# Kernel tuning notes

Hardware: AMD Instinct MI355X
Metric: run time of the kernel (lower is better)

The kernel has to match this reference:

```python
import jax, jax.numpy as jnp
import numpy as np

ALPHA = 1.0
BETA = 0.25
NUM_EMBEDS = 8192
EMBED_DIM = 512
B, T = 32, 256


def setup_inputs() -> dict:
    key = jax.random.key(0)
    k1, k2 = jax.random.split(key)
    z_e = jax.random.normal(k1, (B, EMBED_DIM, T), dtype=jnp.float32)
    codebook = jax.random.normal(k2, (NUM_EMBEDS, EMBED_DIM), dtype=jnp.float32)
    return {"z_e": z_e, "codebook": codebook}


def reference(z_e, codebook):
    # z_e: (b, d, t) -> (b, t, d)
    z = jnp.transpose(z_e, (0, 2, 1))
    b, t, d = z.shape
    flat = z.reshape(-1, d)  # (N, d), N = b*t

    # squared euclidean distances to every codebook vector: (N, K)
    dists = (
        jnp.sum(flat * flat, axis=1, keepdims=True)
        + jnp.sum(codebook * codebook, axis=1)
        - 2.0 * flat @ codebook.T
    )
    idx = jnp.argmin(dists, axis=1)  # (N,)

    # codebook lookup (equivalent to one-hot @ codebook)
    z_q = codebook[idx].reshape(b, t, d)

    # commitment loss (codebook is EMA-updated, so only e_latent term)
    e_latent_loss = jnp.mean((jax.lax.stop_gradient(z_q) - z) ** 2)
    vq_loss = ALPHA * BETA * e_latent_loss

    # straight-through estimator
    z_q_st = z + jax.lax.stop_gradient(z_q - z)
    z_q_out = jnp.transpose(z_q_st, (0, 2, 1))  # back to (b, d, t)

    # perplexity from mean one-hot assignment probabilities
    counts = jnp.zeros((codebook.shape[0],), dtype=jnp.float32).at[idx].add(1.0)
    avg_probs = counts / flat.shape[0]
    perplexity = jnp.exp(-jnp.sum(avg_probs * jnp.log(avg_probs + 1e-10)))

    return z_q_out, vq_loss, perplexity
```

## Files before the change

kernel.cpp:

```cpp
#include <hip/hip_runtime.h>
#include <stdint.h>

typedef _Float16 half8 __attribute__((ext_vector_type(8)));
typedef float floatx16 __attribute__((ext_vector_type(16)));
typedef unsigned long long u64;

#define ALPHA_ 1.0f
#define BETA_ 0.25f
#define NUM_EMBEDS 8192
#define EMBED_DIM 512
#define B_ 32
#define T_ 256
#define N_TOK 8192
#define THR_GAP 2e-3f


__device__ __forceinline__ uint32_t mono(float s) {
    uint32_t u = __float_as_uint(s);
    return (u & 0x80000000u) ? ~u : (u | 0x80000000u);
}
__device__ __forceinline__ float unmono(uint32_t v) {
    return __uint_as_float((v & 0x80000000u) ? (v ^ 0x80000000u) : ~v);
}

__global__ void pack_cb_kernel(const float* __restrict__ cb, _Float16* __restrict__ cf,
                               float* __restrict__ cnorm) {
    int row = blockIdx.x * 4 + (threadIdx.x >> 6);
    int l = threadIdx.x & 63;
    const float* src = cb + (size_t)row * EMBED_DIM + l * 8;
    float4 v0 = *(const float4*)src;
    float4 v1 = *(const float4*)(src + 4);
    float x[8] = {v0.x, v0.y, v0.z, v0.w, v1.x, v1.y, v1.z, v1.w};
    half8 hh, mm;
    float s = 0.f;
#pragma unroll
    for (int j = 0; j < 8; ++j) {
        s += x[j] * x[j];
        _Float16 hv = (_Float16)x[j];
        hh[j] = hv;
        mm[j] = (_Float16)((x[j] - (float)hv) * 2048.0f);
    }
    int s_ = l >> 2, kk = (l >> 1) & 1, hfb = l & 1;
    int slot0 = s_ * 4 + kk * 2;
    size_t base = (size_t)(row >> 5) * 32768 + (size_t)slot0 * 512 +
                  (size_t)((row & 31) + hfb * 32) * 8;
    *(half8*)(cf + base) = hh;
    *(half8*)(cf + base + 512) = mm;
#pragma unroll
    for (int d = 32; d; d >>= 1) s += __shfl_xor(s, d, 64);
    if (l == 0) cnorm[row] = s;
}

__global__ void pack_z_kernel(const float* __restrict__ z, _Float16* __restrict__ zf) {
    int tid = threadIdx.x;
    int l = tid & 63, ds = tid >> 6;
    int n = blockIdx.x * 64 + l;
    int b = n >> 8, t = n & 255;
    int kk = ds >> 1, hfb = ds & 1;
    int tb = n >> 7, q = (n >> 5) & 3;
    size_t lanebase = (size_t)tb * 131072 + (size_t)q * 512 +
                      (size_t)((n & 31) + hfb * 32) * 8;
    for (int g = 0; g < 16; ++g) {
        int d0 = g * 32 + ds * 8;
        const float* src = z + ((size_t)b * EMBED_DIM + d0) * T_ + t;
        half8 hh, mm;
#pragma unroll
        for (int j = 0; j < 8; ++j) {
            float x = -2.0f * src[(size_t)j * T_];
            _Float16 hv = (_Float16)x;
            hh[j] = hv;
            mm[j] = (_Float16)((x - (float)hv) * 2048.0f);
        }
        int slot0 = g * 4 + kk * 2;
        _Float16* dst = zf + lanebase + (size_t)slot0 * 2048;
        *(half8*)dst = hh;
        *(half8*)(dst + 2048) = mm;
    }
}

#define MFMA16(a, b, c) __builtin_amdgcn_mfma_f32_32x32x16_f16(a, b, c, 0, 0, 0)

#define LOADSET(X, hs)                                                              \
    X##Ah = *(const half8*)(Ab + ((hs)*2 + 0) * 512 + lane8);                       \
    X##Am = *(const half8*)(Ab + ((hs)*2 + 1) * 512 + lane8);                       \
    _Pragma("unroll") for (int q_ = 0; q_ < 4; ++q_) {                              \
        X##Bh[q_] = *(const half8*)(Bb + (((hs)*2 + 0) * 4 + q_) * 512 + lane8);    \
        X##Bm[q_] = *(const half8*)(Bb + (((hs)*2 + 1) * 4 + q_) * 512 + lane8);    \
    }

#define MFMASET(X)                                                                  \
    _Pragma("unroll") for (int q_ = 0; q_ < 4; ++q_)                                \
        acc1[q_] = MFMA16(X##Ah, X##Bh[q_], acc1[q_]);                              \
    _Pragma("unroll") for (int q_ = 0; q_ < 4; ++q_)                                \
        acc2[q_] = MFMA16(X##Ah, X##Bm[q_], acc2[q_]);                              \
    _Pragma("unroll") for (int q_ = 0; q_ < 4; ++q_)                                \
        acc2[q_] = MFMA16(X##Am, X##Bh[q_], acc2[q_]);

__global__ __launch_bounds__(512, 2) void argmin_kernel(
    const _Float16* __restrict__ cb_f, const _Float16* __restrict__ zt_f,
    const float* __restrict__ cnorm, u64* __restrict__ slot_m1,
    _Float16* __restrict__ slot_d) {
    __shared__ u64 sK[8][128];
    __shared__ float sV1[8][128], sV2[8][128];

    const int tid = threadIdx.x;
    const int l = tid & 63;
    const int wv = tid >> 6;
    const int l31 = l & 31;
    const int hf = l >> 5;
    const int tb = blockIdx.x;
    const int c0 = blockIdx.y * 256;
    const int cb32 = blockIdx.y * 8 + wv;

    const _Float16* Ab = cb_f + (size_t)cb32 * 32768;
    const _Float16* Bb = zt_f + (size_t)tb * 131072;
    const int lane8 = l * 8;

    floatx16 acc1[4], acc2[4];
#pragma unroll
    for (int q = 0; q < 4; ++q)
#pragma unroll
        for (int r = 0; r < 16; ++r) { acc1[q][r] = 0.f; acc2[q][r] = 0.f; }

    half8 cAh, cAm, cBh[4], cBm[4];
    half8 nAh, nAm, nBh[4], nBm[4];

    LOADSET(c, 0);
    for (int hs = 0; hs < 30; hs += 2) {
        LOADSET(n, hs + 1);
        MFMASET(c);
        LOADSET(c, hs + 2);
        MFMASET(n);
    }
    LOADSET(n, 31);
    MFMASET(c);
    MFMASET(n);

    const int cb0 = c0 + wv * 32;
    u64 km[4]; float kv1[4], kv2[4];
#pragma unroll
    for (int q = 0; q < 4; ++q) {
        u64 m1k = ~0ULL;
        float m1v = 3.4e38f, m2 = 3.4e38f;
#pragma unroll
        for (int g = 0; g < 4; ++g) {
            const int cb4 = cb0 + g * 8 + hf * 4;
            float4 cn = *(const float4*)(cnorm + cb4);
            float sv[4] = {cn.x + acc1[q][g * 4 + 0] + acc2[q][g * 4 + 0] * (1.0f / 2048.0f),
                           cn.y + acc1[q][g * 4 + 1] + acc2[q][g * 4 + 1] * (1.0f / 2048.0f),
                           cn.z + acc1[q][g * 4 + 2] + acc2[q][g * 4 + 2] * (1.0f / 2048.0f),
                           cn.w + acc1[q][g * 4 + 3] + acc2[q][g * 4 + 3] * (1.0f / 2048.0f)};
#pragma unroll
            for (int r = 0; r < 4; ++r) {
                u64 key = ((u64)mono(sv[r]) << 32) | (uint32_t)(cb4 + r);
                if (key < m1k) { m2 = m1v; m1v = sv[r]; m1k = key; }
                else m2 = fminf(m2, sv[r]);
            }
        }
        u64 ok = __shfl_xor(m1k, 32, 64);
        float ov = __shfl_xor(m1v, 32, 64);
        float om2 = __shfl_xor(m2, 32, 64);
        if (ok < m1k) { m2 = fminf(fminf(m2, om2), m1v); m1v = ov; m1k = ok; }
        else m2 = fminf(fminf(m2, om2), ov);
        km[q] = m1k; kv1[q] = m1v; kv2[q] = m2;
    }
    if (hf == 0) {
#pragma unroll
        for (int q = 0; q < 4; ++q) {
            int idx = q * 32 + l31;
            sK[wv][idx] = km[q]; sV1[wv][idx] = kv1[q]; sV2[wv][idx] = kv2[q];
        }
    }
    __syncthreads();
    if (tid < 128) {
        u64 m1k = ~0ULL;
        float m1v = 3.4e38f, m2 = 3.4e38f;
#pragma unroll
        for (int w = 0; w < 8; ++w) {
            u64 ok = sK[w][tid]; float ov = sV1[w][tid], om2 = sV2[w][tid];
            if (ok < m1k) { m2 = fminf(fminf(m2, om2), m1v); m1v = ov; m1k = ok; }
            else m2 = fminf(fminf(m2, om2), ov);
        }
        int tok = tb * 128 + tid;
        slot_m1[((size_t)blockIdx.y << 13) + tok] = m1k;
        slot_d[((size_t)blockIdx.y << 13) + tok] = (_Float16)(m2 - m1v);
    }
}

__global__ void combine_kernel(const u64* __restrict__ slot_m1, const _Float16* __restrict__ slot_d,
                               u64* __restrict__ wexact, int* __restrict__ worklist,
                               int* __restrict__ nflag) {
    int tok = blockIdx.x * 256 + threadIdx.x;
    u64 g1 = ~0ULL;
    float g1v = 3.4e38f, g2 = 3.4e38f;
    for (int c = 0; c < 32; ++c) {
        u64 k = slot_m1[((size_t)c << 13) + tok];
        float kv = unmono((uint32_t)(k >> 32));
        float v2 = kv + (float)slot_d[((size_t)c << 13) + tok];
        if (k < g1) { g2 = fminf(g2, g1v); g1 = k; g1v = kv; }
        else g2 = fminf(g2, kv);
        g2 = fminf(g2, v2);
    }
    if (g2 - g1v > THR_GAP) wexact[tok] = g1;
    else { int i = atomicAdd(nflag, 1); if (i < 8192) worklist[i] = tok; }
}

__global__ void fallback_kernel(const float* __restrict__ z, const float* __restrict__ cb,
                                const float* __restrict__ cnorm,
                                const int* __restrict__ worklist, const int* __restrict__ nflag,
                                u64* __restrict__ wexact) {
    int n = *nflag;
    if (n > 8192) n = 8192;
    const int l = threadIdx.x & 63, wv = threadIdx.x >> 6;
    const int cbase = blockIdx.x * 128;
    for (int fi = blockIdx.y; fi < n; fi += gridDim.y) {
        int tok = worklist[fi];
        int b = tok >> 8, t = tok & 255;
        const float* zp = z + ((size_t)b * EMBED_DIM) * T_ + t;
        float zr[8];
#pragma unroll
        for (int j = 0; j < 8; ++j) zr[j] = zp[(size_t)(l * 8 + j) * T_];
        u64 m1 = ~0ULL;
        for (int j = 0; j < 32; ++j) {
            int c = cbase + wv + j * 4;
            const float* cp = cb + (size_t)c * EMBED_DIM + l * 8;
            float4 a = *(const float4*)cp, bb = *(const float4*)(cp + 4);
            float dot = zr[0] * a.x + zr[1] * a.y + zr[2] * a.z + zr[3] * a.w +
                        zr[4] * bb.x + zr[5] * bb.y + zr[6] * bb.z + zr[7] * bb.w;
#pragma unroll
            for (int m = 32; m; m >>= 1) dot += __shfl_xor(dot, m, 64);
            if (l == 0) {
                float s = cnorm[c] - 2.0f * dot;
                u64 key = ((u64)mono(s) << 32) | (uint32_t)c;
                if (key < m1) m1 = key;
            }
        }
        if (l == 0) atomicMin(&wexact[tok], m1);
    }
}

__global__ void gather_kernel(const float* __restrict__ z, const float* __restrict__ cb,
                              const u64* __restrict__ wexact,
                              float* __restrict__ out, int* __restrict__ counts,
                              float* __restrict__ sse_acc) {
    __shared__ unsigned int sIdx[64];
    __shared__ float red[4];
    const int tid = threadIdx.x;
    const int n0 = blockIdx.x * 64;
    const int b = n0 >> 8;
    const int t0 = n0 & 255;
    if (tid < 64) {
        unsigned int idx = (unsigned int)(wexact[n0 + tid] & 0xffffffffULL);
        sIdx[tid] = idx;
        atomicAdd(&counts[idx], 1);
    }
    __syncthreads();
    const int w = tid >> 6;
    const int lane = tid & 63;
    const float* crow = cb + (size_t)sIdx[lane] * EMBED_DIM;
    const size_t base = ((size_t)b * EMBED_DIM) * T_ + (size_t)(t0 + lane);
    float sse = 0.f;
    for (int d = w; d < EMBED_DIM; d += 4) {
        float v = crow[d];
        size_t o = base + (size_t)d * T_;
        float diff = v - z[o];
        out[o] = v;
        sse += diff * diff;
    }
    for (int m = 32; m; m >>= 1) sse += __shfl_xor(sse, m, 64);
    if (lane == 0) red[w] = sse;
    __syncthreads();
    if (tid == 0) atomicAdd(sse_acc, red[0] + red[1] + red[2] + red[3]);
}

__global__ void finalize_kernel(const int* __restrict__ counts,
                                const float* __restrict__ sse_acc,
                                float* __restrict__ out) {
    __shared__ float red[4];
    const int tid = threadIdx.x;
    float e = 0.f;
    for (int k = tid; k < NUM_EMBEDS; k += 256) {
        float p = (float)counts[k] * (1.0f / (float)N_TOK);
        e += p * logf(p + 1e-10f);
    }
    for (int m = 32; m; m >>= 1) e += __shfl_xor(e, m, 64);
    if ((tid & 63) == 0) red[tid >> 6] = e;
    __syncthreads();
    if (tid == 0) {
        float ent = red[0] + red[1] + red[2] + red[3];
        size_t off = (size_t)B_ * EMBED_DIM * T_;
        out[off + 0] = (ALPHA_ * BETA_) * sse_acc[0] / (float)((size_t)N_TOK * EMBED_DIM);
        out[off + 1] = expf(-ent);
    }
}

extern "C" void kernel_launch(void* const* d_in, const int* in_sizes, int n_in,
                              void* d_out, int out_size, void* d_ws, size_t ws_size,
                              hipStream_t stream) {
    const float* z = (const float*)d_in[0];
    const float* cb = (const float*)d_in[1];
    float* out = (float*)d_out;
    char* ws = (char*)d_ws;
    u64* wexact = (u64*)ws;
    float* cnorm = (float*)(ws + 65536);
    int* counts = (int*)(ws + 98304);
    float* sse = (float*)(ws + 131072);
    int* nflag = (int*)(ws + 131076);
    int* worklist = (int*)(ws + 131080);
    u64* slot_m1 = (u64*)(ws + (1ull << 20));
    _Float16* slot_d = (_Float16*)(ws + (5ull << 20));
    _Float16* cb_f = (_Float16*)(ws + (6ull << 20));
    _Float16* zt_f = (_Float16*)(ws + (22ull << 20));

    hipMemsetAsync(wexact, 0xFF, NUM_EMBEDS * sizeof(u64), stream);
    hipMemsetAsync(counts, 0, NUM_EMBEDS * sizeof(int) + 8, stream);

    pack_cb_kernel<<<NUM_EMBEDS / 4, 256, 0, stream>>>(cb, cb_f, cnorm);
    pack_z_kernel<<<N_TOK / 64, 256, 0, stream>>>(z, zt_f);
    argmin_kernel<<<dim3(N_TOK / 128, NUM_EMBEDS / 256), 512, 0, stream>>>(cb_f, zt_f, cnorm, slot_m1, slot_d);
    combine_kernel<<<N_TOK / 256, 256, 0, stream>>>(slot_m1, slot_d, wexact, worklist, nflag);
    fallback_kernel<<<dim3(64, 16), 256, 0, stream>>>(z, cb, cnorm, worklist, nflag, wexact);
    gather_kernel<<<N_TOK / 64, 256, 0, stream>>>(z, cb, wexact, out, counts, sse);
    finalize_kernel<<<1, 256, 0, stream>>>(counts, sse, out);
}
```

Baseline: 373.2 us.

## Drop fp16 split-precision residual MFMAs and use norm-based error bound with pruned fallback

New measurement: 560.1 us. 50.1% more time.

```diff
diff --git a/kernel.cpp b/kernel.cpp
--- a/kernel.cpp
+++ b/kernel.cpp
@@ -12,7 +12,6 @@
 #define B_ 32
 #define T_ 256
 #define N_TOK 8192
-#define THR_GAP 2e-3f
 
 
 __device__ __forceinline__ uint32_t mono(float s) {
@@ -24,176 +23,147 @@
 }
 
 __global__ void pack_cb_kernel(const float* __restrict__ cb, _Float16* __restrict__ cf,
-                               float* __restrict__ cnorm) {
+                               float* __restrict__ cnorm, unsigned int* __restrict__ maxC2) {
     int row = blockIdx.x * 4 + (threadIdx.x >> 6);
     int l = threadIdx.x & 63;
     const float* src = cb + (size_t)row * EMBED_DIM + l * 8;
     float4 v0 = *(const float4*)src;
     float4 v1 = *(const float4*)(src + 4);
     float x[8] = {v0.x, v0.y, v0.z, v0.w, v1.x, v1.y, v1.z, v1.w};
-    half8 hh, mm;
+    half8 hh;
     float s = 0.f;
 #pragma unroll
     for (int j = 0; j < 8; ++j) {
         s += x[j] * x[j];
-        _Float16 hv = (_Float16)x[j];
-        hh[j] = hv;
-        mm[j] = (_Float16)((x[j] - (float)hv) * 2048.0f);
-    }
-    int s_ = l >> 2, kk = (l >> 1) & 1, hfb = l & 1;
-    int slot0 = s_ * 4 + kk * 2;
-    size_t base = (size_t)(row >> 5) * 32768 + (size_t)slot0 * 512 +
-                  (size_t)((row & 31) + hfb * 32) * 8;
-    *(half8*)(cf + base) = hh;
-    *(half8*)(cf + base + 512) = mm;
+        hh[j] = (_Float16)x[j];
+    }
+    int slot = (l >> 2) * 2 + ((l >> 1) & 1);
+    int flane = (row & 31) + (l & 1) * 32;
+    *(half8*)(cf + (size_t)(row >> 5) * 16384 + (size_t)slot * 512 + flane * 8) = hh;
 #pragma unroll
     for (int d = 32; d; d >>= 1) s += __shfl_xor(s, d, 64);
-    if (l == 0) cnorm[row] = s;
-}
-
-__global__ void pack_z_kernel(const float* __restrict__ z, _Float16* __restrict__ zf) {
+    if (l == 0) {
+        cnorm[row] = s;
+        atomicMax(maxC2, __float_as_uint(s));
+    }
+}
+
+__global__ void pack_z_kernel(const float* __restrict__ z, _Float16* __restrict__ zf,
+                              float* __restrict__ znorm) {
     int tid = threadIdx.x;
     int l = tid & 63, ds = tid >> 6;
     int n = blockIdx.x * 64 + l;
     int b = n >> 8, t = n & 255;
     int kk = ds >> 1, hfb = ds & 1;
     int tb = n >> 7, q = (n >> 5) & 3;
-    size_t lanebase = (size_t)tb * 131072 + (size_t)q * 512 +
+    size_t lanebase = (size_t)tb * 65536 + (size_t)q * 512 +
                       (size_t)((n & 31) + hfb * 32) * 8;
+    float zz = 0.f;
     for (int g = 0; g < 16; ++g) {
         int d0 = g * 32 + ds * 8;
         const float* src = z + ((size_t)b * EMBED_DIM + d0) * T_ + t;
-        half8 hh, mm;
+        half8 hh;
 #pragma unroll
         for (int j = 0; j < 8; ++j) {
-            float x = -2.0f * src[(size_t)j * T_];
-            _Float16 hv = (_Float16)x;
-            hh[j] = hv;
-            mm[j] = (_Float16)((x - (float)hv) * 2048.0f);
+            float zo = src[(size_t)j * T_];
+            zz += zo * zo;
+            hh[j] = (_Float16)(-2.0f * zo);
         }
-        int slot0 = g * 4 + kk * 2;
-        _Float16* dst = zf + lanebase + (size_t)slot0 * 2048;
-        *(half8*)dst = hh;
-        *(half8*)(dst + 2048) = mm;
-    }
+        int slot = g * 2 + kk;
+        *(half8*)(zf + lanebase + (size_t)slot * 2048) = hh;
+    }
+    atomicAdd(&znorm[n], zz);
 }
 
 #define MFMA16(a, b, c) __builtin_amdgcn_mfma_f32_32x32x16_f16(a, b, c, 0, 0, 0)
 
-#define LOADSET(X, hs)                                                              \
-    X##Ah = *(const half8*)(Ab + ((hs)*2 + 0) * 512 + lane8);                       \
-    X##Am = *(const half8*)(Ab + ((hs)*2 + 1) * 512 + lane8);                       \
-    _Pragma("unroll") for (int q_ = 0; q_ < 4; ++q_) {                              \
-        X##Bh[q_] = *(const half8*)(Bb + (((hs)*2 + 0) * 4 + q_) * 512 + lane8);    \
-        X##Bm[q_] = *(const half8*)(Bb + (((hs)*2 + 1) * 4 + q_) * 512 + lane8);    \
-    }
-
-#define MFMASET(X)                                                                  \
-    _Pragma("unroll") for (int q_ = 0; q_ < 4; ++q_)                                \
-        acc1[q_] = MFMA16(X##Ah, X##Bh[q_], acc1[q_]);                              \
-    _Pragma("unroll") for (int q_ = 0; q_ < 4; ++q_)                                \
-        acc2[q_] = MFMA16(X##Ah, X##Bm[q_], acc2[q_]);                              \
-    _Pragma("unroll") for (int q_ = 0; q_ < 4; ++q_)                                \
-        acc2[q_] = MFMA16(X##Am, X##Bh[q_], acc2[q_]);
-
-__global__ __launch_bounds__(512, 2) void argmin_kernel(
-    const _Float16* __restrict__ cb_f, const _Float16* __restrict__ zt_f,
+#define LDSET(s, hs)                                                  \
+    fr[s][0] = *(const half8*)(Ab0 + (hs) * 512 + l8);                \
+    fr[s][1] = *(const half8*)(Ab1 + (hs) * 512 + l8);                \
+    fr[s][2] = *(const half8*)(Bb + (hs) * 2048 + 0 * 512 + l8);      \
+    fr[s][3] = *(const half8*)(Bb + (hs) * 2048 + 1 * 512 + l8);      \
+    fr[s][4] = *(const half8*)(Bb + (hs) * 2048 + 2 * 512 + l8);      \
+    fr[s][5] = *(const half8*)(Bb + (hs) * 2048 + 3 * 512 + l8);
+
+__global__ __launch_bounds__(256, 2) void argmin_kernel(
+    const _Float16* __restrict__ cb_h, const _Float16* __restrict__ zt_h,
     const float* __restrict__ cnorm, u64* __restrict__ slot_m1,
     _Float16* __restrict__ slot_d) {
-    __shared__ u64 sK[8][128];
-    __shared__ float sV1[8][128], sV2[8][128];
-
     const int tid = threadIdx.x;
     const int l = tid & 63;
     const int wv = tid >> 6;
     const int l31 = l & 31;
     const int hf = l >> 5;
-    const int tb = blockIdx.x;
-    const int c0 = blockIdx.y * 256;
-    const int cb32 = blockIdx.y * 8 + wv;
-
-    const _Float16* Ab = cb_f + (size_t)cb32 * 32768;
-    const _Float16* Bb = zt_f + (size_t)tb * 131072;
-    const int lane8 = l * 8;
-
-    floatx16 acc1[4], acc2[4];
-#pragma unroll
-    for (int q = 0; q < 4; ++q)
-#pragma unroll
-        for (int r = 0; r < 16; ++r) { acc1[q][r] = 0.f; acc2[q][r] = 0.f; }
-
-    half8 cAh, cAm, cBh[4], cBm[4];
-    half8 nAh, nAm, nBh[4], nBm[4];
-
-    LOADSET(c, 0);
-    for (int hs = 0; hs < 30; hs += 2) {
-        LOADSET(n, hs + 1);
-        MFMASET(c);
-        LOADSET(c, hs + 2);
-        MFMASET(n);
-    }
-    LOADSET(n, 31);
-    MFMASET(c);
-    MFMASET(n);
-
-    const int cb0 = c0 + wv * 32;
-    u64 km[4]; float kv1[4], kv2[4];
+    const int cid = blockIdx.y * 4 + wv;
+    const _Float16* Ab0 = cb_h + (size_t)(cid * 2) * 16384;
+    const _Float16* Ab1 = Ab0 + 16384;
+    const _Float16* Bb = zt_h + (size_t)blockIdx.x * 65536;
+    const int l8 = l * 8;
+
+    floatx16 acc[2][4];
+#pragma unroll
+    for (int a = 0; a < 2; ++a)
+#pragma unroll
+        for (int q = 0; q < 4; ++q)
+#pragma unroll
+            for (int r = 0; r < 16; ++r) acc[a][q][r] = 0.f;
+
+    half8 fr[3][6];
+    LDSET(0, 0)
+    LDSET(1, 1)
+#pragma unroll
+    for (int t = 0; t < 32; ++t) {
+        const int s = t % 3;
+        if (t + 2 < 32) {
+            LDSET((t + 2) % 3, t + 2)
+        }
+#pragma unroll
+        for (int q = 0; q < 4; ++q) acc[0][q] = MFMA16(fr[s][0], fr[s][2 + q], acc[0][q]);
+#pragma unroll
+        for (int q = 0; q < 4; ++q) acc[1][q] = MFMA16(fr[s][1], fr[s][2 + q], acc[1][q]);
+    }
+
+    const int cb0 = cid * 64;
 #pragma unroll
     for (int q = 0; q < 4; ++q) {
         u64 m1k = ~0ULL;
         float m1v = 3.4e38f, m2 = 3.4e38f;
 #pragma unroll
-        for (int g = 0; g < 4; ++g) {
-            const int cb4 = cb0 + g * 8 + hf * 4;
-            float4 cn = *(const float4*)(cnorm + cb4);
-            float sv[4] = {cn.x + acc1[q][g * 4 + 0] + acc2[q][g * 4 + 0] * (1.0f / 2048.0f),
-                           cn.y + acc1[q][g * 4 + 1] + acc2[q][g * 4 + 1] * (1.0f / 2048.0f),
-                           cn.z + acc1[q][g * 4 + 2] + acc2[q][g * 4 + 2] * (1.0f / 2048.0f),
-                           cn.w + acc1[q][g * 4 + 3] + acc2[q][g * 4 + 3] * (1.0f / 2048.0f)};
-#pragma unroll
-            for (int r = 0; r < 4; ++r) {
-                u64 key = ((u64)mono(sv[r]) << 32) | (uint32_t)(cb4 + r);
-                if (key < m1k) { m2 = m1v; m1v = sv[r]; m1k = key; }
-                else m2 = fminf(m2, sv[r]);
+        for (int ti = 0; ti < 2; ++ti)
+#pragma unroll
+            for (int g = 0; g < 4; ++g) {
+                const int cb4 = cb0 + ti * 32 + g * 8 + hf * 4;
+                float4 cn = *(const float4*)(cnorm + cb4);
+                float sv[4] = {cn.x + acc[ti][q][g * 4 + 0], cn.y + acc[ti][q][g * 4 + 1],
+                               cn.z + acc[ti][q][g * 4 + 2], cn.w + acc[ti][q][g * 4 + 3]};
+#pragma unroll
+                for (int r = 0; r < 4; ++r) {
+                    u64 key = ((u64)mono(sv[r]) << 32) | (uint32_t)(cb4 + r);
+                    if (key < m1k) { m2 = m1v; m1v = sv[r]; m1k = key; }
+                    else m2 = fminf(m2, sv[r]);
+                }
             }
-        }
         u64 ok = __shfl_xor(m1k, 32, 64);
         float ov = __shfl_xor(m1v, 32, 64);
         float om2 = __shfl_xor(m2, 32, 64);
         if (ok < m1k) { m2 = fminf(fminf(m2, om2), m1v); m1v = ov; m1k = ok; }
         else m2 = fminf(fminf(m2, om2), ov);
-        km[q] = m1k; kv1[q] = m1v; kv2[q] = m2;
-    }
-    if (hf == 0) {
-#pragma unroll
-        for (int q = 0; q < 4; ++q) {
-            int idx = q * 32 + l31;
-            sK[wv][idx] = km[q]; sV1[wv][idx] = kv1[q]; sV2[wv][idx] = kv2[q];
+        if (hf == 0) {
+            int tok = blockIdx.x * 128 + q * 32 + l31;
+            slot_m1[((size_t)cid << 13) + tok] = m1k;
+            slot_d[((size_t)cid << 13) + tok] = (_Float16)(m2 - m1v);
         }
     }
-    __syncthreads();
-    if (tid < 128) {
-        u64 m1k = ~0ULL;
-        float m1v = 3.4e38f, m2 = 3.4e38f;
-#pragma unroll
-        for (int w = 0; w < 8; ++w) {
-            u64 ok = sK[w][tid]; float ov = sV1[w][tid], om2 = sV2[w][tid];
-            if (ok < m1k) { m2 = fminf(fminf(m2, om2), m1v); m1v = ov; m1k = ok; }
-            else m2 = fminf(fminf(m2, om2), ov);
-        }
-        int tok = tb * 128 + tid;
-        slot_m1[((size_t)blockIdx.y << 13) + tok] = m1k;
-        slot_d[((size_t)blockIdx.y << 13) + tok] = (_Float16)(m2 - m1v);
-    }
 }
 
 __global__ void combine_kernel(const u64* __restrict__ slot_m1, const _Float16* __restrict__ slot_d,
+                               const float* __restrict__ znorm, const unsigned int* __restrict__ maxC2,
                                u64* __restrict__ wexact, int* __restrict__ worklist,
-                               int* __restrict__ nflag) {
+                               int* __restrict__ nflag, float* __restrict__ cut) {
     int tok = blockIdx.x * 256 + threadIdx.x;
     u64 g1 = ~0ULL;
     float g1v = 3.4e38f, g2 = 3.4e38f;
-    for (int c = 0; c < 32; ++c) {
+    for (int c = 0; c < 128; ++c) {
         u64 k = slot_m1[((size_t)c << 13) + tok];
         float kv = unmono((uint32_t)(k >> 32));
         float v2 = kv + (float)slot_d[((size_t)c << 13) + tok];
@@ -201,41 +171,52 @@
         else g2 = fminf(g2, kv);
         g2 = fminf(g2, v2);
     }
-    if (g2 - g1v > THR_GAP) wexact[tok] = g1;
-    else { int i = atomicAdd(nflag, 1); if (i < 8192) worklist[i] = tok; }
+    float maxC = sqrtf(__uint_as_float(*maxC2));
+    float thr = sqrtf(znorm[tok]) * maxC * (1.0f / 256.0f) + 0.15f;
+    if (g2 - g1v > thr) wexact[tok] = g1;
+    else {
+        int i = atomicAdd(nflag, 1);
+        if (i < 8192) worklist[i] = tok;
+        cut[tok] = g1v + thr;
+    }
 }
 
 __global__ void fallback_kernel(const float* __restrict__ z, const float* __restrict__ cb,
                                 const float* __restrict__ cnorm,
                                 const int* __restrict__ worklist, const int* __restrict__ nflag,
+                                const u64* __restrict__ slot_m1, const float* __restrict__ cut,
                                 u64* __restrict__ wexact) {
     int n = *nflag;
     if (n > 8192) n = 8192;
     const int l = threadIdx.x & 63, wv = threadIdx.x >> 6;
-    const int cbase = blockIdx.x * 128;
-    for (int fi = blockIdx.y; fi < n; fi += gridDim.y) {
+    for (int fi = blockIdx.x; fi < n; fi += gridDim.x) {
         int tok = worklist[fi];
         int b = tok >> 8, t = tok & 255;
         const float* zp = z + ((size_t)b * EMBED_DIM) * T_ + t;
         float zr[8];
 #pragma unroll
         for (int j = 0; j < 8; ++j) zr[j] = zp[(size_t)(l * 8 + j) * T_];
+        float cutv = cut[tok];
         u64 m1 = ~0ULL;
-        for (int j = 0; j < 32; ++j) {
-            int c = cbase + wv + j * 4;
-            const float* cp = cb + (size_t)c * EMBED_DIM + l * 8;
-            float4 a = *(const float4*)cp, bb = *(const float4*)(cp + 4);
-            float dot = zr[0] * a.x + zr[1] * a.y + zr[2] * a.z + zr[3] * a.w +
-                        zr[4] * bb.x + zr[5] * bb.y + zr[6] * bb.z + zr[7] * bb.w;
-#pragma unroll
-            for (int m = 32; m; m >>= 1) dot += __shfl_xor(dot, m, 64);
-            if (l == 0) {
-                float s = cnorm[c] - 2.0f * dot;
-                u64 key = ((u64)mono(s) << 32) | (uint32_t)c;
-                if (key < m1) m1 = key;
+        for (int cid = wv; cid < 128; cid += 4) {
+            u64 sk = slot_m1[((size_t)cid << 13) + tok];
+            if (unmono((uint32_t)(sk >> 32)) > cutv) continue;
+            for (int j = 0; j < 64; ++j) {
+                int c = cid * 64 + j;
+                const float* cp = cb + (size_t)c * EMBED_DIM + l * 8;
+                float4 a = *(const float4*)cp, bb = *(const float4*)(cp + 4);
+                float dot = zr[0] * a.x + zr[1] * a.y + zr[2] * a.z + zr[3] * a.w +
+                            zr[4] * bb.x + zr[5] * bb.y + zr[6] * bb.z + zr[7] * bb.w;
+#pragma unroll
+                for (int m = 32; m; m >>= 1) dot += __shfl_xor(dot, m, 64);
+                if (l == 0) {
+                    float s = cnorm[c] - 2.0f * dot;
+                    u64 key = ((u64)mono(s) << 32) | (uint32_t)c;
+                    if (key < m1) m1 = key;
+                }
             }
         }
-        if (l == 0) atomicMin(&wexact[tok], m1);
+        if (l == 0 && m1 != ~0ULL) atomicMin(&wexact[tok], m1);
     }
 }
 
@@ -304,22 +285,25 @@
     u64* wexact = (u64*)ws;
     float* cnorm = (float*)(ws + 65536);
     int* counts = (int*)(ws + 98304);
-    float* sse = (float*)(ws + 131072);
-    int* nflag = (int*)(ws + 131076);
-    int* worklist = (int*)(ws + 131080);
+    float* znorm = (float*)(ws + 131072);
+    float* sse = (float*)(ws + 163840);
+    int* nflag = (int*)(ws + 163844);
+    unsigned int* maxC2 = (unsigned int*)(ws + 163848);
+    int* worklist = (int*)(ws + 163856);
+    float* cut = (float*)(ws + 196624);
     u64* slot_m1 = (u64*)(ws + (1ull << 20));
-    _Float16* slot_d = (_Float16*)(ws + (5ull << 20));
-    _Float16* cb_f = (_Float16*)(ws + (6ull << 20));
-    _Float16* zt_f = (_Float16*)(ws + (22ull << 20));
+    _Float16* slot_d = (_Float16*)(ws + (9ull << 20));
+    _Float16* cb_h = (_Float16*)(ws + (10ull << 20));
+    _Float16* zt_h = (_Float16*)(ws + (18ull << 20));
 
     hipMemsetAsync(wexact, 0xFF, NUM_EMBEDS * sizeof(u64), stream);
-    hipMemsetAsync(counts, 0, NUM_EMBEDS * sizeof(int) + 8, stream);
-
-    pack_cb_kernel<<<NUM_EMBEDS / 4, 256, 0, stream>>>(cb, cb_f, cnorm);
-    pack_z_kernel<<<N_TOK / 64, 256, 0, stream>>>(z, zt_f);
-    argmin_kernel<<<dim3(N_TOK / 128, NUM_EMBEDS / 256), 512, 0, stream>>>(cb_f, zt_f, cnorm, slot_m1, slot_d);
-    combine_kernel<<<N_TOK / 256, 256, 0, stream>>>(slot_m1, slot_d, wexact, worklist, nflag);
-    fallback_kernel<<<dim3(64, 16), 256, 0, stream>>>(z, cb, cnorm, worklist, nflag, wexact);
+    hipMemsetAsync(counts, 0, 65536 + 12, stream);
+
+    pack_cb_kernel<<<NUM_EMBEDS / 4, 256, 0, stream>>>(cb, cb_h, cnorm, maxC2);
+    pack_z_kernel<<<N_TOK / 64, 256, 0, stream>>>(z, zt_h, znorm);
+    argmin_kernel<<<dim3(N_TOK / 128, 32), 256, 0, stream>>>(cb_h, zt_h, cnorm, slot_m1, slot_d);
+    combine_kernel<<<N_TOK / 256, 256, 0, stream>>>(slot_m1, slot_d, znorm, maxC2, wexact, worklist, nflag, cut);
+    fallback_kernel<<<1024, 256, 0, stream>>>(z, cb, cnorm, worklist, nflag, slot_m1, cut, wexact);
     gather_kernel<<<N_TOK / 64, 256, 0, stream>>>(z, cb, wexact, out, counts, sse);
     finalize_kernel<<<1, 256, 0, stream>>>(counts, sse, out);
 }
```
